# Optimization experiments

Hardware: AMD Instinct MI355X
Metric: run time of the kernel (lower is better)

Reference implementation:

```python
import jax, jax.numpy as jnp
import numpy as np

B, S, D, H = 8, 1024, 1024, 16
HD = D // H
EPS = 1e-06


def setup_inputs() -> dict:
    key = jax.random.key(0)
    ks = jax.random.split(key, 10)
    sc = 0.02
    inp = {
        "y": jax.random.normal(ks[0], (B, S, D), dtype=jnp.float32),
        "y_mask": jax.random.randint(ks[1], (B, 1, 1, S), 0, 2) == 1,
        "Wq": jax.random.normal(ks[2], (D, D), dtype=jnp.float32) * sc,
        "bq": jnp.zeros((D,), jnp.float32),
        "Wk": jax.random.normal(ks[3], (D, D), dtype=jnp.float32) * sc,
        "bk": jnp.zeros((D,), jnp.float32),
        "Wv": jax.random.normal(ks[4], (D, D), dtype=jnp.float32) * sc,
        "bv": jnp.zeros((D,), jnp.float32),
        "Wm": jax.random.normal(ks[5], (D, D), dtype=jnp.float32) * sc,
        "bm": jnp.zeros((D,), jnp.float32),
        "a2": jnp.ones((D,), jnp.float32),
        "b2": jnp.zeros((D,), jnp.float32),
    }
    return inp


def _heads(x):
    # [B,S,D] -> [B,H,S,HD]
    return x.reshape(B, S, H, HD).transpose(0, 2, 1, 3)


def reference(y, y_mask, Wq, bq, Wk, bk, Wv, bv, Wm, bm, a2, b2):
    # torch Linear: x @ W^T + b
    q = _heads(y @ Wq.T + bq)
    k = _heads(y @ Wk.T + bk)
    v = _heads(y @ Wv.T + bv)
    scores = jnp.einsum("bhqd,bhkd->bhqk", q, k) / jnp.sqrt(jnp.float32(HD))
    scores = jnp.where(y_mask, jnp.float32(-1e9), scores)
    att = jax.nn.softmax(scores, axis=-1)  # dropout = identity in eval
    atted = jnp.einsum("bhqk,bhkd->bhqd", att, v)
    atted = atted.transpose(0, 2, 1, 3).reshape(B, S, D)
    atted = atted @ Wm.T + bm
    x = y + atted  # residual (dropout1 = identity in eval)
    mean = x.mean(-1, keepdims=True)
    # torch std: unbiased (ddof=1); eps added to std, not variance
    std = jnp.sqrt(((x - mean) ** 2).sum(-1, keepdims=True) / jnp.float32(D - 1))
    return a2 * (x - mean) / (std + EPS) + b2
```

## Files before the change

### kernel.cpp

```cpp
#include <hip/hip_runtime.h>

#define DEVFN __device__ __forceinline__

typedef unsigned short u16;
typedef __attribute__((ext_vector_type(8))) unsigned short u16x8;
typedef __attribute__((ext_vector_type(4))) unsigned short u16x4;
typedef __attribute__((ext_vector_type(8))) __bf16 bf16x8;
typedef __attribute__((ext_vector_type(4))) float f32x4;

DEVFN u16 f2bf_hw(float f) {
    return __builtin_bit_cast(u16, (__bf16)f);
}

DEVFN float bf2f(u16 h) {
    unsigned u = (unsigned)h << 16;
    return __builtin_bit_cast(float, u);
}

DEVFN bf16x8 ldfrag(const u16* p) {
    return __builtin_bit_cast(bf16x8, *(const u16x8*)p);
}

DEVFN f32x4 mfma16(bf16x8 a, bf16x8 b, f32x4 c) {
    return __builtin_amdgcn_mfma_f32_16x16x32_bf16(a, b, c, 0, 0, 0);
}

DEVFN void async16(const u16* g, u16* l) {
    __builtin_amdgcn_global_load_lds(
        (const __attribute__((address_space(1))) void*)g,
        (__attribute__((address_space(3))) void*)l, 16, 0, 0);
}

__global__ __launch_bounds__(256) void conv_all(const float* __restrict__ y,
                                                const float* __restrict__ w0,
                                                const float* __restrict__ w1,
                                                const float* __restrict__ w2,
                                                const float* __restrict__ w3,
                                                u16* __restrict__ yb,
                                                u16* __restrict__ wb,
                                                const int* __restrict__ mask,
                                                int* __restrict__ idx,
                                                int* __restrict__ cnt) {
    const int b = blockIdx.x;
    if (b >= 12288) {
        const int wave = threadIdx.x >> 6, lane = threadIdx.x & 63;
        for (int bb = wave; bb < 8; bb += 4) {
            const int* m = mask + bb * 1024;
            int* ib = idx + bb * 1024;
            int base = 0;
            for (int t = 0; t < 16; ++t) {
                const int pos = t * 64 + lane;
                const int valid = (m[pos] == 0) ? 1 : 0;
                const unsigned long long bal = __ballot(valid);
                const int pre = __popcll(bal & ((1ull << lane) - 1ull));
                if (valid) ib[base + pre] = pos;
                base += (int)__popcll(bal);
            }
            if (lane == 0) cnt[bb] = base;
            for (int i = base + lane; i < 1024; i += 64) ib[i] = 0;
        }
        return;
    }
    const float* src;
    u16* dst;
    int i;
    if (b < 8192) {
        src = y; dst = yb;
        i = b * 1024 + threadIdx.x * 4;
    } else {
        const int g = (b - 8192) >> 10;
        src = g == 0 ? w0 : (g == 1 ? w1 : (g == 2 ? w2 : w3));
        dst = wb + (size_t)g * 1024 * 1024;
        i = ((b - 8192) & 1023) * 1024 + threadIdx.x * 4;
    }
    const float4 v = *(const float4*)&src[i];
    u16x4 o;
    o.x = f2bf_hw(v.x); o.y = f2bf_hw(v.y);
    o.z = f2bf_hw(v.z); o.w = f2bf_hw(v.w);
    *(u16x4*)&dst[i] = o;
}

__global__ __launch_bounds__(512, 2) void gemm_qkv(const u16* __restrict__ A,
                                                   const u16* __restrict__ Wq,
                                                   const u16* __restrict__ Wkv,
                                                   const float* __restrict__ bq,
                                                   const float* __restrict__ bk,
                                                   const float* __restrict__ bv,
                                                   u16* __restrict__ qb,
                                                   u16* __restrict__ kb,
                                                   u16* __restrict__ vb,
                                                   const int* __restrict__ idxb,
                                                   const int* __restrict__ cntb) {
    const int K = 1024;
    __shared__ u16 lds[2][24576];
    const int tid = threadIdx.x;
    const int wave = tid >> 6, lane = tid & 63;
    const int quad = lane >> 4, l16 = lane & 15;
    const int wm = wave >> 1, wn = wave & 1;
    const int cpx = gridDim.x >> 3;
    const int sb = (blockIdx.x & 7) * cpx + (blockIdx.x >> 3);
    int m0, n0, rowbase;
    const u16* Bt;
    const float *bp0, *bp1;
    u16 *cp0, *cp1;
    const int* ib = nullptr;
    if (sb < 256) {
        m0 = (sb >> 3) * 256;
        n0 = (sb & 7) * 128;
        rowbase = 0;
        Bt = Wq; bp0 = bq; bp1 = bq; cp0 = qb; cp1 = qb;
    } else {
        const int t = sb - 256;
        const int nb = t & 15, mb = (t >> 4) & 3, b = t >> 6;
        const int cn = cntb[b];
        const int pc = (cn + 255) & ~255;
        m0 = mb * 256;
        if (m0 >= pc) return;
        n0 = nb * 128;
        rowbase = b * 1024;
        ib = idxb + b * 1024;
        Bt = Wkv; bp0 = bk; bp1 = bv; cp0 = kb; cp1 = vb;
    }
    const int sr = lane >> 3, sc = lane & 7;
    const int scs = (sc ^ sr) << 3;
    const int ar = m0 + wave * 8 + sr;
    int r0 = ar, r1 = ar + 64, r2 = ar + 128, r3 = ar + 192;
    if (ib) { r0 = ib[r0]; r1 = ib[r1]; r2 = ib[r2]; r3 = ib[r3]; }
    const u16* As0 = A + (size_t)(rowbase + r0) * K + scs;
    const u16* As1 = A + (size_t)(rowbase + r1) * K + scs;
    const u16* As2 = A + (size_t)(rowbase + r2) * K + scs;
    const u16* As3 = A + (size_t)(rowbase + r3) * K + scs;
    const u16* Bs0 = Bt + (size_t)(n0 + wave * 8 + sr) * K + scs;
    const u16* Bs1 = Bs0 + (size_t)64 * K;
    const int swz = (quad ^ (l16 & 7)) << 3;
    const int rofA = (wm * 64 + l16) * 64 + swz;
    const int rofB = (wn * 64 + l16) * 64 + swz;

#define STA(off, bf)                                           \
    do {                                                       \
        async16(As0 + (off), &lds[bf][0] + wave * 512);        \
        async16(As1 + (off), &lds[bf][4096] + wave * 512);     \
        async16(As2 + (off), &lds[bf][8192] + wave * 512);     \
        async16(As3 + (off), &lds[bf][12288] + wave * 512);    \
    } while (0)
#define STB(off, bf)                                           \
    do {                                                       \
        async16(Bs0 + (off), &lds[bf][16384] + wave * 512);    \
        async16(Bs1 + (off), &lds[bf][20480] + wave * 512);    \
    } while (0)

    f32x4 acc[4][4] = {};
    const int NT = K >> 6;

    STA(0, 0);
    STB(0, 0);
    STA(64, 1);
    asm volatile("s_waitcnt vmcnt(4)" ::: "memory");
    __builtin_amdgcn_s_barrier();

    for (int t = 0; t < NT; ++t) {
        const int buf = t & 1;
        const u16* Ar = &lds[buf][0];
        const u16* Br = &lds[buf][16384];
        bf16x8 af[4][2], bfr[4][2];
        #pragma unroll
        for (int mi = 0; mi < 4; ++mi) {
            af[mi][0] = ldfrag(Ar + mi * 1024 + rofA);
            af[mi][1] = ldfrag(Ar + mi * 1024 + (rofA ^ 32));
        }
        #pragma unroll
        for (int ni = 0; ni < 2; ++ni) {
            bfr[ni][0] = ldfrag(Br + ni * 1024 + rofB);
            bfr[ni][1] = ldfrag(Br + ni * 1024 + (rofB ^ 32));
        }
        if (t + 1 < NT) STB((t + 1) * 64, buf ^ 1);
        __builtin_amdgcn_s_barrier();
        asm volatile("s_waitcnt lgkmcnt(0)" ::: "memory");
        __builtin_amdgcn_s_setprio(1);
        #pragma unroll
        for (int mi = 0; mi < 4; ++mi)
            #pragma unroll
            for (int ni = 0; ni < 2; ++ni) {
                acc[mi][ni] = mfma16(af[mi][0], bfr[ni][0], acc[mi][ni]);
                acc[mi][ni] = mfma16(af[mi][1], bfr[ni][1], acc[mi][ni]);
            }
        __builtin_amdgcn_s_setprio(0);
        __builtin_amdgcn_s_barrier();
        #pragma unroll
        for (int ni = 2; ni < 4; ++ni) {
            bfr[ni][0] = ldfrag(Br + ni * 1024 + rofB);
            bfr[ni][1] = ldfrag(Br + ni * 1024 + (rofB ^ 32));
        }
        if (t + 2 < NT) STA((t + 2) * 64, buf);
        __builtin_amdgcn_s_barrier();
        asm volatile("s_waitcnt lgkmcnt(0)" ::: "memory");
        __builtin_amdgcn_s_setprio(1);
        #pragma unroll
        for (int mi = 0; mi < 4; ++mi)
            #pragma unroll
            for (int ni = 2; ni < 4; ++ni) {
                acc[mi][ni] = mfma16(af[mi][0], bfr[ni][0], acc[mi][ni]);
                acc[mi][ni] = mfma16(af[mi][1], bfr[ni][1], acc[mi][ni]);
            }
        __builtin_amdgcn_s_setprio(0);
        if (t < NT - 2)
            asm volatile("s_waitcnt vmcnt(4)" ::: "memory");
        else
            asm volatile("s_waitcnt vmcnt(0)" ::: "memory");
        __builtin_amdgcn_s_barrier();
    }
#undef STA
#undef STB
    const int wrow = m0 + wm * 64 + quad * 4;
    #pragma unroll
    for (int ni = 0; ni < 4; ++ni) {
        const int col = n0 + wn * 64 + ni * 16 + l16;
        const int cs = col >> 10;
        const int c = col & 1023;
        const float* bp = cs == 0 ? bp0 : bp1;
        u16* cp = cs == 0 ? cp0 : cp1;
        const float bb = bp[c];
        #pragma unroll
        for (int mi = 0; mi < 4; ++mi)
            #pragma unroll
            for (int r = 0; r < 4; ++r) {
                const int row = rowbase + wrow + mi * 16 + r;
                cp[(size_t)row * 1024 + c] = f2bf_hw(acc[mi][ni][r] + bb);
            }
    }
}

__global__ __launch_bounds__(512, 2) void gemm8b(const u16* __restrict__ A,
                                                 const u16* __restrict__ Bt,
                                                 const float* __restrict__ b0,
                                                 const float* __restrict__ b1,
                                                 const float* __restrict__ b2,
                                                 u16* __restrict__ C0,
                                                 u16* __restrict__ C1,
                                                 u16* __restrict__ C2,
                                                 int K, int NBX) {
    __shared__ u16 lds[2][24576];
    const int NT = K >> 6;
    const int tid = threadIdx.x;
    const int wave = tid >> 6, lane = tid & 63;
    const int quad = lane >> 4, l16 = lane & 15;
    const int wm = wave >> 1, wn = wave & 1;
    const int nwg = gridDim.x, cpx = nwg >> 3;
    const int sb = (blockIdx.x & 7) * cpx + (blockIdx.x >> 3);
    const int bx = sb % NBX, by = sb / NBX;
    const int m0 = by * 256, n0 = bx * 128;
    const int sr = lane >> 3, sc = lane & 7;
    const int scs = (sc ^ sr) << 3;
    const u16* Ag = A + (size_t)(m0 + wave * 8 + sr) * K + scs;
    const u16* Bg = Bt + (size_t)(n0 + wave * 8 + sr) * K + scs;
    const size_t rstep = (size_t)64 * K;
    const int swz = (quad ^ (l16 & 7)) << 3;
    const int rofA = (wm * 64 + l16) * 64 + swz;
    const int rofB = (wn * 64 + l16) * 64 + swz;

#define STAGE(gp, lp)                                        \
    do {                                                     \
        async16((gp), (lp) + wave * 512);                    \
        async16((gp) + rstep, (lp) + 4096 + wave * 512);     \
    } while (0)

    f32x4 acc[4][4] = {};

    STAGE(Ag, &lds[0][0]);
    STAGE(Ag + 2 * rstep, &lds[0][8192]);
    STAGE(Bg, &lds[0][16384]);
    STAGE(Ag + 64, &lds[1][0]);
    STAGE(Ag + 2 * rstep + 64, &lds[1][8192]);
    asm volatile("s_waitcnt vmcnt(4)" ::: "memory");
    __builtin_amdgcn_s_barrier();

    for (int t = 0; t < NT; ++t) {
        const int buf = t & 1;
        const u16* Ar = &lds[buf][0];
        const u16* Br = &lds[buf][16384];
        bf16x8 af[4][2], bfr[4][2];
        #pragma unroll
        for (int mi = 0; mi < 4; ++mi) {
            af[mi][0] = ldfrag(Ar + mi * 1024 + rofA);
            af[mi][1] = ldfrag(Ar + mi * 1024 + (rofA ^ 32));
        }
        #pragma unroll
        for (int ni = 0; ni < 2; ++ni) {
            bfr[ni][0] = ldfrag(Br + ni * 1024 + rofB);
            bfr[ni][1] = ldfrag(Br + ni * 1024 + (rofB ^ 32));
        }
        if (t + 1 < NT) STAGE(Bg + (t + 1) * 64, &lds[buf ^ 1][16384]);
        __builtin_amdgcn_s_barrier();
        asm volatile("s_waitcnt lgkmcnt(0)" ::: "memory");
        __builtin_amdgcn_s_setprio(1);
        #pragma unroll
        for (int mi = 0; mi < 4; ++mi)
            #pragma unroll
            for (int ni = 0; ni < 2; ++ni) {
                acc[mi][ni] = mfma16(af[mi][0], bfr[ni][0], acc[mi][ni]);
                acc[mi][ni] = mfma16(af[mi][1], bfr[ni][1], acc[mi][ni]);
            }
        __builtin_amdgcn_s_setprio(0);
        __builtin_amdgcn_s_barrier();
        #pragma unroll
        for (int ni = 2; ni < 4; ++ni) {
            bfr[ni][0] = ldfrag(Br + ni * 1024 + rofB);
            bfr[ni][1] = ldfrag(Br + ni * 1024 + (rofB ^ 32));
        }
        if (t + 2 < NT) {
            STAGE(Ag + (t + 2) * 64, &lds[buf][0]);
            STAGE(Ag + 2 * rstep + (t + 2) * 64, &lds[buf][8192]);
        }
        __builtin_amdgcn_s_barrier();
        asm volatile("s_waitcnt lgkmcnt(0)" ::: "memory");
        __builtin_amdgcn_s_setprio(1);
        #pragma unroll
        for (int mi = 0; mi < 4; ++mi)
            #pragma unroll
            for (int ni = 2; ni < 4; ++ni) {
                acc[mi][ni] = mfma16(af[mi][0], bfr[ni][0], acc[mi][ni]);
                acc[mi][ni] = mfma16(af[mi][1], bfr[ni][1], acc[mi][ni]);
            }
        __builtin_amdgcn_s_setprio(0);
        if (t < NT - 2)
            asm volatile("s_waitcnt vmcnt(4)" ::: "memory");
        else
            asm volatile("s_waitcnt vmcnt(0)" ::: "memory");
        __builtin_amdgcn_s_barrier();
    }
#undef STAGE
    const int wrow = m0 + wm * 64 + quad * 4;
    #pragma unroll
    for (int ni = 0; ni < 4; ++ni) {
        const int col = n0 + wn * 64 + ni * 16 + l16;
        const int cs = col >> 10;
        const int c = col & 1023;
        const float* bp = cs == 0 ? b0 : (cs == 1 ? b1 : b2);
        u16* cp = cs == 0 ? C0 : (cs == 1 ? C1 : C2);
        const float bb = bp[c];
        #pragma unroll
        for (int mi = 0; mi < 4; ++mi)
            #pragma unroll
            for (int r = 0; r < 4; ++r) {
                const int row = wrow + mi * 16 + r;
                cp[(size_t)row * 1024 + c] = f2bf_hw(acc[mi][ni][r] + bb);
            }
    }
}

__global__ __launch_bounds__(256) void attn(const u16* __restrict__ qb,
                                            const u16* __restrict__ kb,
                                            const u16* __restrict__ vb,
                                            const int* __restrict__ cntb,
                                            u16* __restrict__ attb) {
    const int lin = blockIdx.x;
    const int xcd = lin & 7, slot = lin >> 3;
    const int bh = xcd * 16 + (slot >> 3);
    const int q0 = (slot & 7) * 128;
    const int bb = bh >> 4, h = bh & 15;
    const int tid = threadIdx.x, wave = tid >> 6, lane = tid & 63;
    const int quad = lane >> 4, l16 = lane & 15;
    __shared__ u16 lK[64 * 72];
    __shared__ u16 lV[64 * 72];
    __shared__ u16 lP[128 * 72];

    const int cn = cntb[bb];
    const int kEnd = (cn + 63) & ~63;

    bf16x8 aq[2][2];
    #pragma unroll
    for (int rg = 0; rg < 2; ++rg) {
        const int qrow = q0 + wave * 32 + rg * 16 + l16;
        const u16* qp = qb + (size_t)(bb * 1024 + qrow) * 1024 + h * 64 + quad * 8;
        aq[rg][0] = ldfrag(qp);
        aq[rg][1] = ldfrag(qp + 32);
    }

    f32x4 o[2][4] = {};
    float ps_acc[2][4] = {};

    const int srow = tid >> 3, scol = (tid & 7) * 8;
    const u16* kbase = kb + (size_t)(bb * 1024) * 1024 + h * 64 + scol;
    const u16* vbase = vb + (size_t)(bb * 1024) * 1024 + h * 64 + scol;

    u16x8 nk0 = *(const u16x8*)(kbase + (size_t)srow * 1024);
    u16x8 nk1 = *(const u16x8*)(kbase + (size_t)(srow + 32) * 1024);
    u16x8 nv0 = *(const u16x8*)(vbase + (size_t)srow * 1024);
    u16x8 nv1 = *(const u16x8*)(vbase + (size_t)(srow + 32) * 1024);

    const float C = 0.18033688011112043f;

    for (int kt = 0; kt < kEnd; kt += 64) {
        __syncthreads();
        *(u16x8*)&lK[srow * 72 + scol] = nk0;
        *(u16x8*)&lK[(srow + 32) * 72 + scol] = nk1;
        #pragma unroll
        for (int j = 0; j < 8; ++j) {
            lV[(scol + j) * 72 + srow] = nv0[j];
            lV[(scol + j) * 72 + srow + 32] = nv1[j];
        }
        __syncthreads();
        const int ktn = kt + 64;
        if (ktn < kEnd) {
            nk0 = *(const u16x8*)(kbase + (size_t)(ktn + srow) * 1024);
            nk1 = *(const u16x8*)(kbase + (size_t)(ktn + srow + 32) * 1024);
            nv0 = *(const u16x8*)(vbase + (size_t)(ktn + srow) * 1024);
            nv1 = *(const u16x8*)(vbase + (size_t)(ktn + srow + 32) * 1024);
        }

        bf16x8 kf[4][2];
        #pragma unroll
        for (int n = 0; n < 4; ++n) {
            kf[n][0] = ldfrag(&lK[(n * 16 + l16) * 72 + quad * 8]);
            kf[n][1] = ldfrag(&lK[(n * 16 + l16) * 72 + 32 + quad * 8]);
        }
        f32x4 s[2][4];
        #pragma unroll
        for (int rg = 0; rg < 2; ++rg)
            #pragma unroll
            for (int n = 0; n < 4; ++n) {
                f32x4 t = {};
                t = mfma16(aq[rg][0], kf[n][0], t);
                t = mfma16(aq[rg][1], kf[n][1], t);
                s[rg][n] = t;
            }
        float bias[4];
        #pragma unroll
        for (int n = 0; n < 4; ++n)
            bias[n] = (kt + n * 16 + l16 < cn) ? 0.0f : -1e9f;
        #pragma unroll
        for (int rg = 0; rg < 2; ++rg)
            #pragma unroll
            for (int n = 0; n < 4; ++n)
                #pragma unroll
                for (int r = 0; r < 4; ++r) {
                    const float p =
                        __builtin_amdgcn_exp2f(__builtin_fmaf(s[rg][n][r], C, bias[n]));
                    ps_acc[rg][r] += p;
                    lP[(wave * 32 + rg * 16 + quad * 4 + r) * 72 + n * 16 + l16] =
                        f2bf_hw(p);
                }
        __asm__ __volatile__("s_waitcnt lgkmcnt(0)" ::: "memory");
        bf16x8 ap[2][2];
        #pragma unroll
        for (int rg = 0; rg < 2; ++rg) {
            ap[rg][0] = ldfrag(&lP[(wave * 32 + rg * 16 + l16) * 72 + quad * 8]);
            ap[rg][1] = ldfrag(&lP[(wave * 32 + rg * 16 + l16) * 72 + 32 + quad * 8]);
        }
        bf16x8 vf[4][2];
        #pragma unroll
        for (int ni = 0; ni < 4; ++ni) {
            vf[ni][0] = ldfrag(&lV[(ni * 16 + l16) * 72 + quad * 8]);
            vf[ni][1] = ldfrag(&lV[(ni * 16 + l16) * 72 + 32 + quad * 8]);
        }
        #pragma unroll
        for (int rg = 0; rg < 2; ++rg)
            #pragma unroll
            for (int ni = 0; ni < 4; ++ni) {
                o[rg][ni] = mfma16(ap[rg][0], vf[ni][0], o[rg][ni]);
                o[rg][ni] = mfma16(ap[rg][1], vf[ni][1], o[rg][ni]);
            }
    }
    #pragma unroll
    for (int off = 1; off < 16; off <<= 1)
        #pragma unroll
        for (int rg = 0; rg < 2; ++rg)
            #pragma unroll
            for (int r = 0; r < 4; ++r)
                ps_acc[rg][r] += __shfl_xor(ps_acc[rg][r], off);
    float rl[2][4];
    #pragma unroll
    for (int rg = 0; rg < 2; ++rg)
        #pragma unroll
        for (int r = 0; r < 4; ++r) rl[rg][r] = 1.f / ps_acc[rg][r];
    #pragma unroll
    for (int rg = 0; rg < 2; ++rg)
        #pragma unroll
        for (int ni = 0; ni < 4; ++ni)
            #pragma unroll
            for (int r = 0; r < 4; ++r) {
                const int row = q0 + wave * 32 + rg * 16 + quad * 4 + r;
                attb[(size_t)(bb * 1024 + row) * 1024 + h * 64 + ni * 16 + l16] =
                    f2bf_hw(o[rg][ni][r] * rl[rg][r]);
            }
}

__global__ __launch_bounds__(256) void ln_res(const u16* __restrict__ ybf,
                                              const u16* __restrict__ xpb,
                                              const float* __restrict__ a2,
                                              const float* __restrict__ b2,
                                              float* __restrict__ out) {
    const int row = blockIdx.x, tid = threadIdx.x;
    const size_t base = (size_t)row * 1024;
    const int j = tid * 4;
    const u16x4 yv = *(const u16x4*)&ybf[base + j];
    const u16x4 xv = *(const u16x4*)&xpb[base + j];
    float x[4] = {bf2f(yv.x) + bf2f(xv.x), bf2f(yv.y) + bf2f(xv.y),
                  bf2f(yv.z) + bf2f(xv.z), bf2f(yv.w) + bf2f(xv.w)};
    float s = 0.f, ss = 0.f;
    #pragma unroll
    for (int i = 0; i < 4; ++i) { s += x[i]; ss += x[i] * x[i]; }
    #pragma unroll
    for (int off = 1; off < 64; off <<= 1) {
        s += __shfl_xor(s, off);
        ss += __shfl_xor(ss, off);
    }
    __shared__ float rs[4], rss[4];
    const int wave = tid >> 6, lane = tid & 63;
    if (lane == 0) { rs[wave] = s; rss[wave] = ss; }
    __syncthreads();
    s = rs[0] + rs[1] + rs[2] + rs[3];
    ss = rss[0] + rss[1] + rss[2] + rss[3];
    const float mean = s * (1.f / 1024.f);
    float var = (ss - s * mean) * (1.f / 1023.f);
    var = fmaxf(var, 0.f);
    const float inv = 1.f / (sqrtf(var) + 1e-6f);
    const float4 av = *(const float4*)&a2[j];
    const float4 bv = *(const float4*)&b2[j];
    float4 ov;
    ov.x = av.x * (x[0] - mean) * inv + bv.x;
    ov.y = av.y * (x[1] - mean) * inv + bv.y;
    ov.z = av.z * (x[2] - mean) * inv + bv.z;
    ov.w = av.w * (x[3] - mean) * inv + bv.w;
    *(float4*)&out[base + j] = ov;
}

extern "C" void kernel_launch(void* const* d_in, const int* in_sizes, int n_in,
                              void* d_out, int out_size, void* d_ws, size_t ws_size,
                              hipStream_t stream) {
    (void)in_sizes; (void)n_in; (void)out_size;
    const float* y   = (const float*)d_in[0];
    const int*   msk = (const int*)d_in[1];
    const float* Wq  = (const float*)d_in[2];
    const float* bq  = (const float*)d_in[3];
    const float* Wk  = (const float*)d_in[4];
    const float* bkb = (const float*)d_in[5];
    const float* Wv  = (const float*)d_in[6];
    const float* bv  = (const float*)d_in[7];
    const float* Wm  = (const float*)d_in[8];
    const float* bm  = (const float*)d_in[9];
    const float* a2  = (const float*)d_in[10];
    const float* b2  = (const float*)d_in[11];
    float* out = (float*)d_out;

    char* ws = (char*)d_ws;
    const size_t MB = 1u << 20;
    if (ws_size < 72 * MB) return;
    u16* yb  = (u16*)(ws);
    u16* wqb = (u16*)(ws + 16 * MB);
    u16* wmb = (u16*)(ws + 22 * MB);
    u16* qb  = (u16*)(ws + 24 * MB);
    u16* kb  = (u16*)(ws + 40 * MB);
    u16* vb  = (u16*)(ws + 56 * MB);
    u16* xpb  = qb;

    int* idxb = (int*)d_out;
    int* cntb = idxb + 8192;
    u16* attb = (u16*)((char*)d_out + 16 * MB);

    conv_all<<<12289, 256, 0, stream>>>(y, Wq, Wk, Wv, Wm, yb, wqb,
                                        msk, idxb, cntb);

    gemm_qkv<<<dim3(768), 512, 0, stream>>>(
        yb, wqb, wqb + 1024 * 1024, bq, bkb, bv, qb, kb, vb, idxb, cntb);

    attn<<<dim3(1024), 256, 0, stream>>>(qb, kb, vb, cntb, attb);

    gemm8b<<<dim3(256), 512, 0, stream>>>(
        attb, wmb, bm, bm, bm, xpb, xpb, xpb, 1024, 8);

    ln_res<<<8192, 256, 0, stream>>>(yb, xpb, a2, b2, out);
}
```

Baseline: 265.7 us.

## Single-buffer B tile in QKV GEMM and load all B fragments upfront

The QKV projection GEMM now keeps a single LDS buffer for the B (weight) tile instead of double-buffering it, shrinking shared memory from 96KB to 80KB. All four B fragment pairs are read into registers at the start of each K step, so one barrier/lgkmcnt wait per iteration is removed and the next B tile load is issued after the first MFMA half. This cuts synchronisation and LDS footprint but holds more fragment registers live and exposes more of the B global-load latency, since the next tile must land before the following iteration's reads.

```diff
diff --git a/kernel.cpp b/kernel.cpp
--- a/kernel.cpp
+++ b/kernel.cpp
@@ -92,7 +92,7 @@
                                                    const int* __restrict__ idxb,
                                                    const int* __restrict__ cntb) {
     const int K = 1024;
-    __shared__ u16 lds[2][24576];
+    __shared__ u16 lds[40960];
     const int tid = threadIdx.x;
     const int wave = tid >> 6, lane = tid & 63;
     const int quad = lane >> 4, l16 = lane & 15;
@@ -136,32 +136,32 @@
     const int rofA = (wm * 64 + l16) * 64 + swz;
     const int rofB = (wn * 64 + l16) * 64 + swz;
 
-#define STA(off, bf)                                           \
-    do {                                                       \
-        async16(As0 + (off), &lds[bf][0] + wave * 512);        \
-        async16(As1 + (off), &lds[bf][4096] + wave * 512);     \
-        async16(As2 + (off), &lds[bf][8192] + wave * 512);     \
-        async16(As3 + (off), &lds[bf][12288] + wave * 512);    \
+#define STA(off, bf)                                                  \
+    do {                                                              \
+        async16(As0 + (off), &lds[(bf) * 16384] + wave * 512);        \
+        async16(As1 + (off), &lds[(bf) * 16384 + 4096] + wave * 512); \
+        async16(As2 + (off), &lds[(bf) * 16384 + 8192] + wave * 512); \
+        async16(As3 + (off), &lds[(bf) * 16384 + 12288] + wave * 512);\
     } while (0)
-#define STB(off, bf)                                           \
-    do {                                                       \
-        async16(Bs0 + (off), &lds[bf][16384] + wave * 512);    \
-        async16(Bs1 + (off), &lds[bf][20480] + wave * 512);    \
+#define STB(off)                                           \
+    do {                                                   \
+        async16(Bs0 + (off), &lds[32768] + wave * 512);    \
+        async16(Bs1 + (off), &lds[36864] + wave * 512);    \
     } while (0)
 
     f32x4 acc[4][4] = {};
     const int NT = K >> 6;
 
     STA(0, 0);
-    STB(0, 0);
+    STB(0);
     STA(64, 1);
     asm volatile("s_waitcnt vmcnt(4)" ::: "memory");
     __builtin_amdgcn_s_barrier();
 
     for (int t = 0; t < NT; ++t) {
         const int buf = t & 1;
-        const u16* Ar = &lds[buf][0];
-        const u16* Br = &lds[buf][16384];
+        const u16* Ar = &lds[buf * 16384];
+        const u16* Br = &lds[32768];
         bf16x8 af[4][2], bfr[4][2];
         #pragma unroll
         for (int mi = 0; mi < 4; ++mi) {
@@ -169,11 +169,10 @@
             af[mi][1] = ldfrag(Ar + mi * 1024 + (rofA ^ 32));
         }
         #pragma unroll
-        for (int ni = 0; ni < 2; ++ni) {
+        for (int ni = 0; ni < 4; ++ni) {
             bfr[ni][0] = ldfrag(Br + ni * 1024 + rofB);
             bfr[ni][1] = ldfrag(Br + ni * 1024 + (rofB ^ 32));
         }
-        if (t + 1 < NT) STB((t + 1) * 64, buf ^ 1);
         __builtin_amdgcn_s_barrier();
         asm volatile("s_waitcnt lgkmcnt(0)" ::: "memory");
         __builtin_amdgcn_s_setprio(1);
@@ -186,14 +185,8 @@
             }
         __builtin_amdgcn_s_setprio(0);
         __builtin_amdgcn_s_barrier();
-        #pragma unroll
-        for (int ni = 2; ni < 4; ++ni) {
-            bfr[ni][0] = ldfrag(Br + ni * 1024 + rofB);
-            bfr[ni][1] = ldfrag(Br + ni * 1024 + (rofB ^ 32));
-        }
+        if (t + 1 < NT) STB((t + 1) * 64);
         if (t + 2 < NT) STA((t + 2) * 64, buf);
-        __builtin_amdgcn_s_barrier();
-        asm volatile("s_waitcnt lgkmcnt(0)" ::: "memory");
         __builtin_amdgcn_s_setprio(1);
         #pragma unroll
         for (int mi = 0; mi < 4; ++mi)
```

Measured after the change: 270.7 us. Within noise of the previous version (+1.9%).
